# Performance work log

Hardware: AMD Instinct MI355X
Metric: run time of the kernel (lower is better)

The kernel has to match this reference:

```python
import jax, jax.numpy as jnp
import numpy as np

NUM_GRAPHS = 100
NODES_PER_GRAPH = 500
EDGES_PER_GRAPH = 4000
HIDDEN = 128
RATIO = 0.5


def setup_inputs() -> dict:
    key = jax.random.key(0)
    k1, k2, k3, k4, k5 = jax.random.split(key, 5)
    N = NUM_GRAPHS * NODES_PER_GRAPH
    E = NUM_GRAPHS * EDGES_PER_GRAPH
    emb = jax.random.normal(k1, (N, HIDDEN), dtype=jnp.float32)
    # edges stay within their own graph's node range
    offs = (jnp.arange(NUM_GRAPHS, dtype=jnp.int32) * NODES_PER_GRAPH)[:, None]
    src = jax.random.randint(k2, (NUM_GRAPHS, EDGES_PER_GRAPH), 0, NODES_PER_GRAPH, dtype=jnp.int32) + offs
    dst = jax.random.randint(k3, (NUM_GRAPHS, EDGES_PER_GRAPH), 0, NODES_PER_GRAPH, dtype=jnp.int32) + offs
    edge_index = jnp.stack([src.reshape(-1), dst.reshape(-1)], axis=0)  # [2, E]
    node_batch = jnp.repeat(jnp.arange(NUM_GRAPHS, dtype=jnp.int32), NODES_PER_GRAPH)  # [N]
    s1 = 1.0 / np.sqrt(2 * HIDDEN)
    s2 = 1.0 / np.sqrt(4 * HIDDEN)
    W1 = jax.random.normal(k4, (2 * HIDDEN, 4 * HIDDEN), dtype=jnp.float32) * s1
    b1 = jnp.zeros((4 * HIDDEN,), dtype=jnp.float32)
    W2 = jax.random.normal(k5, (4 * HIDDEN, 1), dtype=jnp.float32) * s2
    b2 = jnp.zeros((1,), dtype=jnp.float32)
    return {"emb": emb, "edge_index": edge_index, "node_batch": node_batch,
            "W1": W1, "b1": b1, "W2": W2, "b2": b2}


def reference(emb, edge_index, node_batch, W1, b1, W2, b2):
    row, col = edge_index[0], edge_index[1]
    E = row.shape[0]
    N = emb.shape[0]

    # --- edge attention: gather endpoint embeddings, concat, 2-layer MLP ---
    edge_rep = jnp.concatenate([emb[row], emb[col]], axis=-1)       # [E, 2H]
    h = jax.nn.relu(edge_rep @ W1 + b1)                              # [E, 4H]
    edge_att = (h @ W2 + b2)[:, 0]                                   # [E]

    # --- per-graph top-k split (split_graph with ratio) ---
    edge_graph = node_batch[row]                                     # [E]
    order = jnp.lexsort((-edge_att, edge_graph))                     # sort by graph, desc score
    counts = jax.ops.segment_sum(jnp.ones(E, jnp.int32), edge_graph,
                                 num_segments=NUM_GRAPHS)            # edges per graph
    offsets = jnp.concatenate([jnp.zeros(1, jnp.int32),
                               jnp.cumsum(counts)[:-1].astype(jnp.int32)])
    g_sorted = edge_graph[order]
    rank = jnp.arange(E, dtype=jnp.int32) - offsets[g_sorted]        # rank within graph
    k_per_graph = jnp.ceil(RATIO * counts.astype(jnp.float32)).astype(jnp.int32)
    causal_sorted = rank < k_per_graph[g_sorted]
    causal_mask = jnp.zeros(E, dtype=bool).at[order].set(causal_sorted)

    causal_edge_weight = jnp.where(causal_mask, edge_att, 0.0)
    spu_edge_weight = jnp.where(causal_mask, 0.0, edge_att)

    # --- relabel: compact node ids for the causal subgraph ---
    cm = causal_mask.astype(jnp.int32)
    deg = jnp.zeros(N, jnp.int32).at[row].add(cm).at[col].add(cm)
    node_mask = deg > 0                                              # nodes kept in causal subgraph
    new_id = jnp.cumsum(node_mask.astype(jnp.int32)) - 1             # compacted ids
    new_row = jnp.where(causal_mask, new_id[row], -1)
    new_col = jnp.where(causal_mask, new_id[col], -1)
    causal_edge_index = jnp.stack([new_row, new_col], axis=0)        # [2, E], -1 = dropped
    causal_x = jnp.where(node_mask[:, None], emb, 0.0)               # masked node features

    return (edge_att, causal_edge_weight, spu_edge_weight,
            causal_mask, causal_edge_index, node_mask, causal_x)
```

## Files before the change

kernel.cpp:

```cpp
#include <hip/hip_runtime.h>
#include <hip/hip_bf16.h>

#define NG      100
#define NPG     500
#define EPG     4000
#define HID     128
#define NNODES  (NG*NPG)
#define NE      (NG*EPG)
#define KSEL    2000
#define NB_SCAN ((NNODES + 255) / 256)

#define MAXB    1024
#define NRC     8
#define RJT     8
#define DELTA   0.03125f

#define O_ATT   0
#define O_CEW   (NE)
#define O_SEW   (2*NE)
#define O_MASK  (3*NE)
#define O_CEI   (4*NE)
#define O_NMASK (6*NE)
#define O_CX    (6*NE + NNODES)

typedef __attribute__((ext_vector_type(8))) short  short8;
typedef __attribute__((ext_vector_type(8))) __bf16 bf16x8;
typedef __attribute__((ext_vector_type(4))) float  f32x4;

#define MFMA16(a,b,c) __builtin_amdgcn_mfma_f32_16x16x32_bf16( \
    __builtin_bit_cast(bf16x8,(a)), __builtin_bit_cast(bf16x8,(b)), (c), 0, 0, 0)

#define GLOAD_LDS16(g, l) __builtin_amdgcn_global_load_lds( \
    (const __attribute__((address_space(1))) unsigned int*)(g), \
    (__attribute__((address_space(3)))       unsigned int*)(l), 16, 0, 0)

__device__ __forceinline__ unsigned short tobf(float x) {
    __hip_bfloat16 hb = __float2bfloat16(x);
    return *(unsigned short*)&hb;
}

#define PREP_TOBF 6250
#define PREP_PACK 512
#define PREP_DEG  49
#define PREP_GRID (PREP_TOBF + PREP_PACK + PREP_DEG + 1)

__global__ __launch_bounds__(256)
void prep_kernel(const float* __restrict__ emb, const float* __restrict__ W1,
                 unsigned short* __restrict__ eb, unsigned short* __restrict__ ph,
                 float* __restrict__ deg, int* __restrict__ bcnt)
{
    const int blk = blockIdx.x;
    const int t   = threadIdx.x;
    if (blk < PREP_TOBF) {
        int i = blk * 256 + t;
        float4 v = ((const float4*)emb)[i];
        ushort4 h;
        h.x = tobf(v.x); h.y = tobf(v.y); h.z = tobf(v.z); h.w = tobf(v.w);
        ((ushort4*)eb)[i] = h;
    } else if (blk < PREP_TOBF + PREP_PACK) {
        int idx  = (blk - PREP_TOBF) * 256 + t;
        int i    = idx & 7;
        int lane = (idx >> 3) & 63;
        int g    = idx >> 9;
        int jsub = g & 3;
        int rem  = g >> 2;
        int jo   = rem & 7;
        int kc   = rem >> 3;
        int j = jo * 64 + jsub * 16 + (lane & 15);
        int k = kc * 32 + (lane >> 4) * 8 + i;
        ph[idx] = tobf(W1[k * 512 + j]);
    } else if (blk < PREP_TOBF + PREP_PACK + PREP_DEG) {
        int i4 = (blk - PREP_TOBF - PREP_PACK) * 256 + t;
        if (i4 < NNODES / 4) ((float4*)deg)[i4] = make_float4(0.f, 0.f, 0.f, 0.f);
    } else {
        if (t < NG) bcnt[t] = 0;
    }
}

#define ATT_EPB  128
#define ATT_GRID (NE / ATT_EPB)

__global__ __launch_bounds__(256)
void att5_kernel(const unsigned short* __restrict__ embb,
                 const unsigned short* __restrict__ w1p,
                 const int* __restrict__ ei,
                 const float* __restrict__ b1,
                 const float* __restrict__ W2,
                 const float* __restrict__ b2,
                 float* __restrict__ out)
{
    __shared__ __align__(16) unsigned short ldsB[16384];

    const int t    = threadIdx.x;
    const int w    = t >> 6;
    const int lane = t & 63;
    const int r16  = lane & 15;
    const int quad = lane >> 4;

    const int e_base = blockIdx.x * ATT_EPB + w * 32;
    const char* eb = (const char*)embb;

    f32x4 A[2][8];
#pragma unroll
    for (int mt = 0; mt < 2; ++mt) {
        int e = min(e_base + mt * 16 + r16, NE - 1);
        const char* sp = eb + (ei[e] << 8);
        const char* dp = eb + (ei[NE + e] << 8);
#pragma unroll
        for (int k4 = 0; k4 < 4; ++k4) {
            A[mt][k4]     = *(const f32x4*)(sp + k4 * 64 + quad * 16);
            A[mt][k4 + 4] = *(const f32x4*)(dp + k4 * 64 + quad * 16);
        }
    }
#pragma unroll
    for (int mt = 0; mt < 2; ++mt)
#pragma unroll
        for (int kc = 0; kc < 8; ++kc)
            asm volatile("" : "+v"(A[mt][kc]));

    float attP[2][4];
#pragma unroll
    for (int mt = 0; mt < 2; ++mt)
#pragma unroll
        for (int rg = 0; rg < 4; ++rg) attP[mt][rg] = 0.0f;

#define STAGE(s_, buf_)                                                      \
    {                                                                        \
        _Pragma("unroll")                                                    \
        for (int cc = 0; cc < 4; ++cc) {                                     \
            int c2   = w * 4 + cc;                                           \
            int kc   = c2 >> 1;                                              \
            int jsub = ((s_) & 1) * 2 + (c2 & 1);                            \
            int jo   = (s_) >> 1;                                            \
            int g    = (kc * 8 + jo) * 4 + jsub;                             \
            GLOAD_LDS16(w1p + g * 512 + lane * 8,                            \
                        ldsB + (buf_) * 8192 + c2 * 512);                    \
        }                                                                    \
    }

    STAGE(0, 0);
    __syncthreads();

    for (int s = 0; s < 16; ++s) {
        const int cur = s & 1;
        if (s < 15) STAGE(s + 1, cur ^ 1);

#pragma unroll
        for (int jsub2 = 0; jsub2 < 2; ++jsub2) {
            f32x4 acc[2];
#pragma unroll
            for (int mt = 0; mt < 2; ++mt) acc[mt] = f32x4{};

#pragma unroll
            for (int kc = 0; kc < 8; ++kc) {
                short8 B = *(const short8*)(ldsB + cur * 8192 +
                                            (kc * 2 + jsub2) * 512 + lane * 8);
#pragma unroll
                for (int mt = 0; mt < 2; ++mt)
                    acc[mt] = MFMA16(A[mt][kc], B, acc[mt]);
            }

            const int j = s * 32 + jsub2 * 16 + r16;
            const float b1v = b1[j], w2v = W2[j];
#pragma unroll
            for (int mt = 0; mt < 2; ++mt)
#pragma unroll
                for (int rg = 0; rg < 4; ++rg)
                    attP[mt][rg] += fmaxf(acc[mt][rg] + b1v, 0.0f) * w2v;
        }
        __syncthreads();
    }
#undef STAGE

#pragma unroll
    for (int mt = 0; mt < 2; ++mt)
#pragma unroll
        for (int rg = 0; rg < 4; ++rg) {
            float v = attP[mt][rg];
#pragma unroll
            for (int msk = 1; msk <= 8; msk <<= 1) v += __shfl_xor(v, msk, 64);
            attP[mt][rg] = v;
        }

    const float bias2 = b2[0];
    if (r16 < 4) {
#pragma unroll
        for (int mt = 0; mt < 2; ++mt) {
            const int row = quad * 4 + r16;
            const int e   = e_base + mt * 16 + row;
            if (e < NE) out[O_ATT + e] = attP[mt][r16] + bias2;
        }
    }
}

__device__ __forceinline__ unsigned enc_key(float f) {
    unsigned u = __float_as_uint(f);
    return (u & 0x80000000u) ? ~u : (u | 0x80000000u);
}
__device__ __forceinline__ float dec_key(unsigned k) {
    unsigned u = (k & 0x80000000u) ? (k ^ 0x80000000u) : ~k;
    return __uint_as_float(u);
}

__device__ __forceinline__ int wave_sum(int c) {
#pragma unroll
    for (int m = 1; m <= 32; m <<= 1) c += __shfl_xor(c, m, 64);
    return c;
}

__global__ __launch_bounds__(256)
void topk4_kernel(const int* __restrict__ ei, float* __restrict__ out,
                  float* __restrict__ deg, int* __restrict__ bcnt,
                  int* __restrict__ need, int* __restrict__ blist)
{
    __shared__ int cnt;

    const int g  = blockIdx.x;
    const int t  = threadIdx.x;
    const int e0 = g * EPG;
    const int cbase = t * 16;
    const bool act = (t < 250);

    unsigned kreg[16];
    if (act) {
#pragma unroll
        for (int q4 = 0; q4 < 4; ++q4) {
            float4 v = *(const float4*)&out[O_ATT + e0 + cbase + q4 * 4];
            kreg[q4 * 4 + 0] = enc_key(v.x);
            kreg[q4 * 4 + 1] = enc_key(v.y);
            kreg[q4 * 4 + 2] = enc_key(v.z);
            kreg[q4 * 4 + 3] = enc_key(v.w);
        }
    }

    unsigned lo = 0u, hi = 0xFFFFFFFFu;
    while (lo < hi) {
        unsigned mid = lo + ((hi - lo) >> 1) + 1u;
        if (t == 0) cnt = 0;
        __syncthreads();
        int c = 0;
        if (act) {
#pragma unroll
            for (int q = 0; q < 16; ++q) c += (kreg[q] >= mid) ? 1 : 0;
        }
        c = wave_sum(c);
        if ((t & 63) == 0 && c) atomicAdd(&cnt, c);
        __syncthreads();
        int f = cnt;
        if (f >= KSEL) lo = mid; else hi = mid - 1u;
        __syncthreads();
    }
    const unsigned K = lo;
    const float v = dec_key(K);
    const unsigned khi = enc_key(v + DELTA);
    const unsigned klo = enc_key(v - DELTA);

    if (t == 0) cnt = 0;
    __syncthreads();
    {
        int c = 0;
        if (act) {
#pragma unroll
            for (int q = 0; q < 16; ++q) c += (kreg[q] > khi) ? 1 : 0;
        }
        c = wave_sum(c);
        if ((t & 63) == 0 && c) atomicAdd(&cnt, c);
    }
    __syncthreads();
    if (t == 0) need[g] = KSEL - cnt;

    if (act) {
#pragma unroll
        for (int q = 0; q < 16; ++q) {
            unsigned kk = kreg[q];
            int ge = e0 + cbase + q;
            float a = dec_key(kk);
            if (kk > khi) {
                out[O_CEW + ge]  = a;
                out[O_SEW + ge]  = 0.0f;
                out[O_MASK + ge] = 1.0f;
                atomicAdd(&deg[ei[ge]], 1.0f);
                atomicAdd(&deg[ei[NE + ge]], 1.0f);
            } else if (kk < klo) {
                out[O_CEW + ge]  = 0.0f;
                out[O_SEW + ge]  = a;
                out[O_MASK + ge] = 0.0f;
            } else {
                int p = atomicAdd(&bcnt[g], 1);
                if (p < MAXB) blist[g * MAXB + p] = ge;
            }
        }
    }
}

#define TE_  128
#define PADX 132
#define PADW 68

__global__ __launch_bounds__(256)
void repair_kernel(const float* __restrict__ emb, const int* __restrict__ ei,
                   const float* __restrict__ W1, const float* __restrict__ b1,
                   const float* __restrict__ W2,
                   const int* __restrict__ bcnt, const int* __restrict__ blist,
                   float* __restrict__ attx8)
{
    const int blk = blockIdx.x;
    const int ch  = blk / (NG * RJT);
    const int rem = blk - ch * (NG * RJT);
    const int g   = rem >> 3;
    const int jt  = rem & 7;
    const int bc  = min(bcnt[g], MAXB);
    if (ch * 128 >= bc) return;

    __shared__ __align__(16) float Xs[32 * PADX];
    __shared__ __align__(16) float Ws[32 * PADW];
    __shared__ int sidx[TE_], cidx[TE_];

    const int t = threadIdx.x;
    if (t < TE_) {
        int lid = ch * 128 + t;
        int lc  = min(lid, bc - 1);
        int e   = blist[g * MAXB + lc];
        sidx[t] = ei[e];
        cidx[t] = ei[NE + e];
    }
    __syncthreads();

    const int te = t & 15;
    const int tj = t >> 4;

    float acc[8][4];
#pragma unroll
    for (int a = 0; a < 8; ++a)
#pragma unroll
        for (int b = 0; b < 4; ++b) acc[a][b] = 0.0f;

    for (int kt = 0; kt < 8; ++kt) {
        __syncthreads();
#pragma unroll
        for (int i = 0; i < 4; ++i) {
            int flat = i * 256 + t;
            int e  = flat >> 3;
            int k4 = flat & 7;
            int k  = kt * 32 + k4 * 4;
            const float* src;
            if (k < HID) src = emb + (long)sidx[e] * HID + k;
            else         src = emb + (long)cidx[e] * HID + (k - HID);
            float4 v = *(const float4*)src;
            int kl = k4 * 4;
            Xs[(kl + 0) * PADX + e] = v.x;
            Xs[(kl + 1) * PADX + e] = v.y;
            Xs[(kl + 2) * PADX + e] = v.z;
            Xs[(kl + 3) * PADX + e] = v.w;
        }
#pragma unroll
        for (int i = 0; i < 2; ++i) {
            int flat = i * 256 + t;
            int kl = flat >> 4;
            int j4 = flat & 15;
            float4 v = *(const float4*)&W1[(kt * 32 + kl) * 512 + jt * 64 + j4 * 4];
            *(float4*)&Ws[kl * PADW + j4 * 4] = v;
        }
        __syncthreads();

#pragma unroll 4
        for (int kl = 0; kl < 32; ++kl) {
            float4 xa = *(const float4*)&Xs[kl * PADX + te * 8];
            float4 xb = *(const float4*)&Xs[kl * PADX + te * 8 + 4];
            float4 wa = *(const float4*)&Ws[kl * PADW + tj * 4];
            float xv[8] = {xa.x, xa.y, xa.z, xa.w, xb.x, xb.y, xb.z, xb.w};
            float wv[4] = {wa.x, wa.y, wa.z, wa.w};
#pragma unroll
            for (int a = 0; a < 8; ++a)
#pragma unroll
                for (int b = 0; b < 4; ++b)
                    acc[a][b] = fmaf(xv[a], wv[b], acc[a][b]);
        }
    }

    const int jb = jt * 64 + tj * 4;
    float4 b1a = *(const float4*)&b1[jb];
    float4 w2a = *(const float4*)&W2[jb];
    float bv[4] = {b1a.x, b1a.y, b1a.z, b1a.w};
    float wv[4] = {w2a.x, w2a.y, w2a.z, w2a.w};
    float attp[8];
#pragma unroll
    for (int a = 0; a < 8; ++a) {
        float s = 0.0f;
#pragma unroll
        for (int b = 0; b < 4; ++b)
            s = fmaf(fmaxf(acc[a][b] + bv[b], 0.0f), wv[b], s);
        attp[a] = s;
    }

    __syncthreads();
    float* red = Xs;
#pragma unroll
    for (int a = 0; a < 8; ++a) red[tj * 136 + te * 8 + a] = attp[a];
    __syncthreads();
    if (t < TE_ && ch * 128 + t < bc) {
        float s = 0.0f;
#pragma unroll
        for (int q = 0; q < 16; ++q) s += red[q * 136 + t];
        attx8[(g * MAXB + ch * 128 + t) * RJT + jt] = s;
    }
}

__global__ __launch_bounds__(256)
void select_kernel(const int* __restrict__ ei, const int* __restrict__ bcnt,
                   const int* __restrict__ need, const int* __restrict__ blist,
                   const float* __restrict__ attx8, const float* __restrict__ b2,
                   float* __restrict__ out, float* __restrict__ deg)
{
    __shared__ float sa[MAXB];
    __shared__ int   si[MAXB];
    const int g = blockIdx.x;
    const int t = threadIdx.x;
    const int b = min(bcnt[g], MAXB);
    const int n = need[g];
    const float bias2 = b2[0];

    for (int i = t; i < b; i += 256) {
        float s = bias2;
#pragma unroll
        for (int jt = 0; jt < RJT; ++jt)
            s += attx8[(g * MAXB + i) * RJT + jt];
        sa[i] = s;
        si[i] = blist[g * MAXB + i];
    }
    __syncthreads();

    for (int i = t; i < b; i += 256) {
        float ai = sa[i];
        int   ii = si[i];
        int rank = 0;
        for (int j = 0; j < b; ++j)
            rank += (sa[j] > ai || (sa[j] == ai && si[j] < ii)) ? 1 : 0;
        bool flag = rank < n;
        out[O_CEW + ii]  = flag ? ai : 0.0f;
        out[O_SEW + ii]  = flag ? 0.0f : ai;
        out[O_MASK + ii] = flag ? 1.0f : 0.0f;
        if (flag) {
            atomicAdd(&deg[ei[ii]], 1.0f);
            atomicAdd(&deg[ei[NE + ii]], 1.0f);
        }
    }
}

__global__ __launch_bounds__(256)
void scanA(const float* __restrict__ deg, int* __restrict__ partials)
{
    __shared__ int s[256];
    int t = threadIdx.x;
    int n = blockIdx.x * 256 + t;
    int m = (n < NNODES && deg[n] > 0.5f) ? 1 : 0;
    s[t] = m;
    __syncthreads();
    for (int off = 128; off > 0; off >>= 1) {
        if (t < off) s[t] += s[t + off];
        __syncthreads();
    }
    if (t == 0) partials[blockIdx.x] = s[0];
}

__global__ __launch_bounds__(256)
void scanB(int* __restrict__ partials)
{
    __shared__ int s[256];
    int t = threadIdx.x;
    int v = (t < NB_SCAN) ? partials[t] : 0;
    s[t] = v;
    __syncthreads();
    for (int off = 1; off < 256; off <<= 1) {
        int x = (t >= off) ? s[t - off] : 0;
        __syncthreads();
        s[t] += x;
        __syncthreads();
    }
    if (t < NB_SCAN) partials[t] = s[t] - v;
}

__global__ __launch_bounds__(256)
void scanC(float* __restrict__ deg_nm, const int* __restrict__ partials,
           int* __restrict__ newid)
{
    __shared__ int s[256];
    int t = threadIdx.x;
    int b = blockIdx.x;
    int n = b * 256 + t;
    int m = (n < NNODES && deg_nm[n] > 0.5f) ? 1 : 0;
    s[t] = m;
    __syncthreads();
    for (int off = 1; off < 256; off <<= 1) {
        int x = (t >= off) ? s[t - off] : 0;
        __syncthreads();
        s[t] += x;
        __syncthreads();
    }
    if (n < NNODES) {
        newid[n]  = partials[b] + s[t] - 1;
        deg_nm[n] = m ? 1.0f : 0.0f;
    }
}

#define FIN_EDGE 1563
#define FIN_GRID (FIN_EDGE + 6250)

__global__ __launch_bounds__(256)
void final_kernel(const float* __restrict__ emb, const int* __restrict__ ei,
                  const int* __restrict__ newid, const float* __restrict__ nm,
                  float* __restrict__ out)
{
    const int blk = blockIdx.x;
    const int t   = threadIdx.x;
    if (blk < FIN_EDGE) {
        int e = blk * 256 + t;
        if (e >= NE) return;
        bool flag = out[O_MASK + e] > 0.5f;
        int row = ei[e];
        int col = ei[NE + e];
        out[O_CEI + e]      = flag ? (float)newid[row] : -1.0f;
        out[O_CEI + NE + e] = flag ? (float)newid[col] : -1.0f;
    } else {
        int i4 = (blk - FIN_EDGE) * 256 + t;
        if (i4 >= NNODES * HID / 4) return;
        int n = i4 >> 5;
        float4 v = ((const float4*)emb)[i4];
        if (!(nm[n] > 0.5f)) v = make_float4(0.0f, 0.0f, 0.0f, 0.0f);
        ((float4*)(out + O_CX))[i4] = v;
    }
}

extern "C" void kernel_launch(void* const* d_in, const int* in_sizes, int n_in,
                              void* d_out, int out_size, void* d_ws, size_t ws_size,
                              hipStream_t stream)
{
    const float* emb = (const float*)d_in[0];
    const int*   ei  = (const int*)d_in[1];
    const float* W1  = (const float*)d_in[3];
    const float* b1  = (const float*)d_in[4];
    const float* W2  = (const float*)d_in[5];
    const float* b2  = (const float*)d_in[6];
    float* out = (float*)d_out;

    char* wsb = (char*)d_ws;
    int*   newid    = (int*)wsb;
    int*   partials = (int*)(wsb + 200704);
    int*   bcnt     = (int*)(wsb + 201728);
    int*   need     = (int*)(wsb + 202752);
    int*   blist    = (int*)(wsb + 203776);
    float* attx8    = (float*)(wsb + 203776 + NG*MAXB*4);
    unsigned short* embb = (unsigned short*)(wsb + 203776 + NG*MAXB*4 + NG*MAXB*RJT*4);
    unsigned short* w1p  = embb + NNODES * HID;
    float* deg = out + O_NMASK;

    prep_kernel<<<PREP_GRID, 256, 0, stream>>>(emb, W1, embb, w1p, deg, bcnt);
    att5_kernel<<<ATT_GRID, 256, 0, stream>>>(embb, w1p, ei, b1, W2, b2, out);
    topk4_kernel<<<NG, 256, 0, stream>>>(ei, out, deg, bcnt, need, blist);
    repair_kernel<<<NG * NRC * RJT, 256, 0, stream>>>(emb, ei, W1, b1, W2,
                                                      bcnt, blist, attx8);
    select_kernel<<<NG, 256, 0, stream>>>(ei, bcnt, need, blist, attx8, b2, out, deg);
    scanA<<<NB_SCAN, 256, 0, stream>>>(deg, partials);
    scanB<<<1, 256, 0, stream>>>(partials);
    scanC<<<NB_SCAN, 256, 0, stream>>>(deg, partials, newid);
    final_kernel<<<FIN_GRID, 256, 0, stream>>>(emb, ei, newid, deg, out);
}
```

Baseline: 387.7 us.

## Stream edge embeddings per K-half instead of holding full A fragments

The edge-attention GEMM no longer keeps all 16 A fragments (both endpoints) resident in registers for the whole kernel. The K dimension is split into source and destination halves. Each stage reloads the matching 4 A fragments from global memory and accumulates 4 output column tiles at once, so the W1 staging layout changes to match. This cuts register pressure to allow higher occupancy, at the cost of re-reading each edge's embeddings 8 times (likely served from cache) and holding more accumulators.

```diff
diff --git a/kernel.cpp b/kernel.cpp
--- a/kernel.cpp
+++ b/kernel.cpp
@@ -100,75 +100,89 @@
     const int e_base = blockIdx.x * ATT_EPB + w * 32;
     const char* eb = (const char*)embb;
 
-    f32x4 A[2][8];
+    int sb[2], db[2];
 #pragma unroll
     for (int mt = 0; mt < 2; ++mt) {
         int e = min(e_base + mt * 16 + r16, NE - 1);
-        const char* sp = eb + (ei[e] << 8);
-        const char* dp = eb + (ei[NE + e] << 8);
-#pragma unroll
-        for (int k4 = 0; k4 < 4; ++k4) {
-            A[mt][k4]     = *(const f32x4*)(sp + k4 * 64 + quad * 16);
-            A[mt][k4 + 4] = *(const f32x4*)(dp + k4 * 64 + quad * 16);
-        }
-    }
+        sb[mt] = ei[e] << 8;
+        db[mt] = ei[NE + e] << 8;
+    }
+
+    float attP[2][4];
 #pragma unroll
     for (int mt = 0; mt < 2; ++mt)
 #pragma unroll
-        for (int kc = 0; kc < 8; ++kc)
-            asm volatile("" : "+v"(A[mt][kc]));
-
-    float attP[2][4];
-#pragma unroll
-    for (int mt = 0; mt < 2; ++mt)
-#pragma unroll
         for (int rg = 0; rg < 4; ++rg) attP[mt][rg] = 0.0f;
 
-#define STAGE(s_, buf_)                                                      \
+#define STAGE(st_, buf_)                                                     \
     {                                                                        \
+        const int jo_ = (st_) >> 1, kh_ = (st_) & 1;                         \
         _Pragma("unroll")                                                    \
         for (int cc = 0; cc < 4; ++cc) {                                     \
-            int c2   = w * 4 + cc;                                           \
-            int kc   = c2 >> 1;                                              \
-            int jsub = ((s_) & 1) * 2 + (c2 & 1);                            \
-            int jo   = (s_) >> 1;                                            \
-            int g    = (kc * 8 + jo) * 4 + jsub;                             \
+            int c    = w * 4 + cc;                                           \
+            int kcl  = c >> 2;                                               \
+            int jsub = c & 3;                                                \
+            int g    = ((kh_ * 4 + kcl) * 8 + jo_) * 4 + jsub;               \
             GLOAD_LDS16(w1p + g * 512 + lane * 8,                            \
-                        ldsB + (buf_) * 8192 + c2 * 512);                    \
+                        ldsB + (buf_) * 8192 + c * 512);                     \
         }                                                                    \
     }
 
     STAGE(0, 0);
     __syncthreads();
 
-    for (int s = 0; s < 16; ++s) {
-        const int cur = s & 1;
-        if (s < 15) STAGE(s + 1, cur ^ 1);
-
-#pragma unroll
-        for (int jsub2 = 0; jsub2 < 2; ++jsub2) {
-            f32x4 acc[2];
-#pragma unroll
-            for (int mt = 0; mt < 2; ++mt) acc[mt] = f32x4{};
-
-#pragma unroll
-            for (int kc = 0; kc < 8; ++kc) {
-                short8 B = *(const short8*)(ldsB + cur * 8192 +
-                                            (kc * 2 + jsub2) * 512 + lane * 8);
+    f32x4 acc[2][4];
+
+    for (int jo = 0; jo < 8; ++jo) {
+#pragma unroll
+        for (int kh = 0; kh < 2; ++kh) {
+            const int st  = jo * 2 + kh;
+            const int cur = st & 1;
+            if (st < 15) STAGE(st + 1, cur ^ 1);
+
+            if (kh == 0) {
 #pragma unroll
                 for (int mt = 0; mt < 2; ++mt)
-                    acc[mt] = MFMA16(A[mt][kc], B, acc[mt]);
+#pragma unroll
+                    for (int js = 0; js < 4; ++js) acc[mt][js] = f32x4{};
             }
 
-            const int j = s * 32 + jsub2 * 16 + r16;
-            const float b1v = b1[j], w2v = W2[j];
-#pragma unroll
-            for (int mt = 0; mt < 2; ++mt)
-#pragma unroll
-                for (int rg = 0; rg < 4; ++rg)
-                    attP[mt][rg] += fmaxf(acc[mt][rg] + b1v, 0.0f) * w2v;
-        }
-        __syncthreads();
+            f32x4 A[2][4];
+#pragma unroll
+            for (int mt = 0; mt < 2; ++mt) {
+                const char* base = eb + (kh ? db[mt] : sb[mt]);
+#pragma unroll
+                for (int kcl = 0; kcl < 4; ++kcl)
+                    A[mt][kcl] = *(const f32x4*)(base + kcl * 64 + quad * 16);
+            }
+
+#pragma unroll
+            for (int jsub = 0; jsub < 4; ++jsub) {
+#pragma unroll
+                for (int kcl = 0; kcl < 4; ++kcl) {
+                    short8 B = *(const short8*)(ldsB + cur * 8192 +
+                                                (kcl * 4 + jsub) * 512 + lane * 8);
+#pragma unroll
+                    for (int mt = 0; mt < 2; ++mt)
+                        acc[mt][jsub] = MFMA16(A[mt][kcl], B, acc[mt][jsub]);
+                }
+            }
+
+            __syncthreads();
+
+            if (kh == 1) {
+#pragma unroll
+                for (int jsub = 0; jsub < 4; ++jsub) {
+                    const int j = jo * 64 + jsub * 16 + r16;
+                    const float b1v = b1[j], w2v = W2[j];
+#pragma unroll
+                    for (int mt = 0; mt < 2; ++mt)
+#pragma unroll
+                        for (int rg = 0; rg < 4; ++rg)
+                            attP[mt][rg] += fmaxf(acc[mt][jsub][rg] + b1v, 0.0f) * w2v;
+                }
+            }
+        }
     }
 #undef STAGE
 
```

New measurement: 396.3 us. 2.2% more time.
